# Performance work log

Measured on AMD Instinct MI355X. Metric: run time of the kernel, lower is better.

Reference implementation:

```python
import jax, jax.numpy as jnp
import numpy as np

IN_FEATURES = 4096
OUT_FEATURES = 768
N_BITS = 8
BATCH = 4096


def setup_inputs() -> dict:
    key = jax.random.key(0)
    k1, k2, k3 = jax.random.split(key, 3)
    latent = jax.random.uniform(k1, (BATCH, IN_FEATURES), dtype=jnp.float32)
    true_sum = jax.random.uniform(k2, (BATCH, OUT_FEATURES * N_BITS), dtype=jnp.float32)
    # kaiming-normal-ish init: std = sqrt(2 / fan_in)
    weight = jax.random.normal(k3, (IN_FEATURES, OUT_FEATURES * N_BITS), dtype=jnp.float32) * np.sqrt(2.0 / IN_FEATURES)
    return {"latent": latent, "true_sum": true_sum, "weight": weight, "n_bits": N_BITS}


def reference(latent, true_sum, weight, n_bits):
    in_features = weight.shape[0]
    batch = latent.shape[0]
    # powers of two, MSB negated (two's-complement style decode)
    powers = (2.0 ** jnp.arange(n_bits, dtype=jnp.float32))
    powers = powers.at[-1].multiply(-1.0)

    prob_weights = jax.nn.sigmoid(weight)                      # [in, out*n_bits]
    # decode soft bits -> integer-valued weights: [in, out]
    int_weights = (prob_weights.reshape(in_features, -1, n_bits) * powers).sum(-1)
    # decode target bits -> integer-valued sums: [batch, out]
    int_sum = (true_sum.reshape(batch, -1, n_bits) * powers).sum(-1)

    # (latent.unsqueeze(-1) * int_weights).sum(-2) is exactly a GEMM
    pred = latent @ int_weights                                # [batch, out]

    scale_factor = 2.0 ** (n_bits - 1)
    recon_loss = jnp.mean((pred - int_sum) ** 2) / scale_factor
    polarize_loss = jnp.mean(prob_weights * (1.0 - prob_weights))
    return (recon_loss, polarize_loss)
```

## Files before the change

kernel.cpp:

```cpp
#include <hip/hip_runtime.h>
#include <stdint.h>

#define IN_F   4096
#define OUT_F  768
#define NB     8
#define BATCH  4096
#define WCOLS  (OUT_F*NB)

typedef short  bf16x8  __attribute__((ext_vector_type(8)));
typedef float  f32x4   __attribute__((ext_vector_type(4)));
typedef unsigned short ushort8 __attribute__((ext_vector_type(8)));

__device__ __forceinline__ unsigned short f2bf(float f){
    union { float f; uint32_t u; } v; v.f = f;
    uint32_t u = v.u;
    u += 0x7FFFu + ((u >> 16) & 1u);
    return (unsigned short)(u >> 16);
}

__device__ __forceinline__ float bf2f(unsigned short u){
    union { uint32_t q; float f; } v; v.q = ((uint32_t)u) << 16;
    return v.f;
}

__device__ __forceinline__ void gload16(const void* g, void* l){
    __builtin_amdgcn_global_load_lds(
        (const __attribute__((address_space(1))) unsigned int*)g,
        (__attribute__((address_space(3))) unsigned int*)l, 16, 0, 0);
}

#define WAITV(n) do {                                                   \
    asm volatile("s_waitcnt vmcnt(" #n ")" ::: "memory");               \
    __builtin_amdgcn_sched_barrier(0);                                  \
} while (0)

__global__ void prep_latent(const float* __restrict__ lat,
                            unsigned short* __restrict__ abf,
                            float* __restrict__ acc){
    if (blockIdx.x == 0 && threadIdx.x < 4) acc[threadIdx.x] = 0.f;
    int idx = (blockIdx.x * 256 + threadIdx.x) * 8;
    const float4* p = (const float4*)(lat + idx);
    float4 a = p[0], b = p[1];
    ushort8 o;
    o[0]=f2bf(a.x); o[1]=f2bf(a.y); o[2]=f2bf(a.z); o[3]=f2bf(a.w);
    o[4]=f2bf(b.x); o[5]=f2bf(b.y); o[6]=f2bf(b.z); o[7]=f2bf(b.w);
    *(ushort8*)(abf + idx) = o;
}

__global__ void decode_weight(const float* __restrict__ w,
                              unsigned short* __restrict__ bt,
                              float* __restrict__ acc){
    __shared__ unsigned short tile[64][70];
    __shared__ float part[4];
    const int tid = threadIdx.x;
    const int k0 = blockIdx.x * 64;
    const int n0 = blockIdx.y * 64;
    const int j     = tid & 63;
    const int ibase = (tid >> 6) * 16;
    float pol = 0.f;
    #pragma unroll 4
    for (int r = 0; r < 16; ++r){
        int i = ibase + r;
        const float4* src = (const float4*)(w + (size_t)(k0+i)*WCOLS + (size_t)(n0+j)*8);
        float4 a = src[0], b = src[1];
        float x[8] = {a.x,a.y,a.z,a.w,b.x,b.y,b.z,b.w};
        float p[8];
        #pragma unroll
        for (int q = 0; q < 8; ++q){
            p[q] = 1.f / (1.f + __expf(-x[q]));
            pol += p[q] * (1.f - p[q]);
        }
        float iw = p[0] + 2.f*p[1] + 4.f*p[2] + 8.f*p[3]
                 + 16.f*p[4] + 32.f*p[5] + 64.f*p[6] - 128.f*p[7];
        tile[j][i] = f2bf(iw);
    }
    #pragma unroll
    for (int off = 32; off; off >>= 1) pol += __shfl_down(pol, off);
    if ((tid & 63) == 0) part[tid >> 6] = pol;
    __syncthreads();
    const int nrow = tid >> 4;
    const int kb   = (tid & 15) * 4;
    #pragma unroll
    for (int q = 0; q < 4; ++q){
        int n = nrow + q*16;
        uint2 v;
        v.x = *(const unsigned int*)&tile[n][kb];
        v.y = *(const unsigned int*)&tile[n][kb+2];
        *(uint2*)(bt + (size_t)(n0+n)*IN_F + k0 + kb) = v;
    }
    if (tid == 0) atomicAdd(&acc[1], part[0]+part[1]+part[2]+part[3]);
}

__global__ void ts_decode(const float* __restrict__ ts,
                          unsigned short* __restrict__ isum){
    const int tid = threadIdx.x;
    #pragma unroll
    for (int k = 0; k < 6; ++k){
        int e = blockIdx.x * 1536 + k * 256 + tid;
        const float4* q = (const float4*)(ts + (size_t)e * 8);
        float4 x = q[0], y = q[1];
        float v = x.x + 2.f*x.y + 4.f*x.z + 8.f*x.w
                + 16.f*y.x + 32.f*y.y + 64.f*y.z - 128.f*y.w;
        isum[e] = f2bf(v);
    }
}

#define BM 64
#define BN 96
#define BK 64
#define NT (IN_F/BK)
#define ABYTES (BM*BK*2)
#define BBYTES (BN*BK*2)
#define BUFB   (ABYTES+BBYTES)

__launch_bounds__(256, 2)
__global__ void gemm_loss(const unsigned short* __restrict__ abf,
                          const unsigned short* __restrict__ bt,
                          const unsigned short* __restrict__ isum,
                          float* __restrict__ acc){
    __shared__ char smem[3*BUFB];
    __shared__ float part[4];
    const int tid = threadIdx.x;
    const int w   = tid >> 6;
    const int l   = tid & 63;
    const int s   = l & 15, g = l >> 4;
    const int wr  = w >> 1, wc = w & 1;
    const int m0  = blockIdx.x * BM;
    const int n0  = blockIdx.y * BN;

    f32x4 accv[2][3];
    #pragma unroll
    for (int m = 0; m < 2; ++m)
        #pragma unroll
        for (int n = 0; n < 3; ++n)
            accv[m][n] = (f32x4){0.f,0.f,0.f,0.f};

    const int c8  = tid & 7;
    const int r0  = tid >> 3;
    const int scw = ((c8 ^ (r0 & 7)) << 3);
    const unsigned short* aS = abf + (size_t)(m0 + r0) * IN_F + scw;
    const unsigned short* bS = bt  + (size_t)(n0 + r0) * IN_F + scw;

    #define STAGE(kt, base) do {                                           \
        const int _ko = (kt) * BK;                                         \
        char* _ad = (base) + tid*16;                                       \
        char* _bd = (base) + ABYTES + tid*16;                              \
        gload16(aS + _ko,                      _ad);                       \
        gload16(aS + (size_t)32*IN_F + _ko,    _ad + 4096);                \
        gload16(bS + _ko,                      _bd);                       \
        gload16(bS + (size_t)32*IN_F + _ko,    _bd + 4096);                \
        gload16(bS + (size_t)64*IN_F + _ko,    _bd + 8192);                \
    } while (0)

    #define COMPUTE(base) do {                                             \
        char* _Ab = (base);                                                \
        char* _Bb = (base) + ABYTES;                                       \
        _Pragma("unroll")                                                  \
        for (int _kk = 0; _kk < 2; ++_kk){                                 \
            bf16x8 _af[2], _bf[3];                                         \
            _Pragma("unroll")                                              \
            for (int _m = 0; _m < 2; ++_m){                                \
                int _r  = wr*32 + _m*16 + s;                               \
                int _ch = _r*8 + ((_kk*4 + g) ^ (_r & 7));                 \
                _af[_m] = *(const bf16x8*)(_Ab + _ch*16);                  \
            }                                                              \
            _Pragma("unroll")                                              \
            for (int _n = 0; _n < 3; ++_n){                                \
                int _r  = wc*48 + _n*16 + s;                               \
                int _ch = _r*8 + ((_kk*4 + g) ^ (_r & 7));                 \
                _bf[_n] = *(const bf16x8*)(_Bb + _ch*16);                  \
            }                                                              \
            _Pragma("unroll")                                              \
            for (int _m = 0; _m < 2; ++_m)                                 \
                _Pragma("unroll")                                          \
                for (int _n = 0; _n < 3; ++_n)                             \
                    accv[_m][_n] = __builtin_amdgcn_mfma_f32_16x16x32_bf16(\
                        _af[_m], _bf[_n], accv[_m][_n], 0, 0, 0);          \
        }                                                                  \
    } while (0)

    char* p0 = smem;
    char* p1 = smem + BUFB;
    char* p2 = smem + 2*BUFB;

    STAGE(0, p0);
    STAGE(1, p1);
    for (int t = 0; t < NT-1; ++t){
        WAITV(5);
        __builtin_amdgcn_s_barrier();
        if (t + 2 < NT) STAGE(t + 2, p2);
        COMPUTE(p0);
        char* tmp = p0; p0 = p1; p1 = p2; p2 = tmp;
    }
    WAITV(0);
    __builtin_amdgcn_s_barrier();
    COMPUTE(p0);

    float local = 0.f;
    #pragma unroll
    for (int m = 0; m < 2; ++m){
        int rbase = m0 + wr*32 + m*16 + g*4;
        #pragma unroll
        for (int n = 0; n < 3; ++n){
            int col = n0 + wc*48 + n*16 + s;
            #pragma unroll
            for (int jj = 0; jj < 4; ++jj){
                float is = bf2f(isum[(size_t)(rbase+jj)*OUT_F + col]);
                float d = accv[m][n][jj] - is;
                local += d*d;
            }
        }
    }
    #pragma unroll
    for (int off = 32; off; off >>= 1) local += __shfl_down(local, off);
    if (l == 0) part[w] = local;
    __syncthreads();
    if (tid == 0){
        atomicAdd(&acc[0], part[0]+part[1]+part[2]+part[3]);
    }
}

__global__ void finalize(const float* __restrict__ acc, float* __restrict__ out){
    out[0] = acc[0] * (1.0f / ((float)BATCH * (float)OUT_F * 128.0f));
    out[1] = acc[1] * (1.0f / ((float)IN_F * (float)WCOLS));
}

extern "C" void kernel_launch(void* const* d_in, const int* in_sizes, int n_in,
                              void* d_out, int out_size, void* d_ws, size_t ws_size,
                              hipStream_t stream){
    const float* latent   = (const float*)d_in[0];
    const float* true_sum = (const float*)d_in[1];
    const float* weight   = (const float*)d_in[2];
    float* acc = (float*)d_ws;
    unsigned short* abf  = (unsigned short*)((char*)d_ws + 1024);
    unsigned short* bt   = (unsigned short*)((char*)d_ws + 1024 + (size_t)BATCH*IN_F*2);
    unsigned short* isum = (unsigned short*)((char*)d_ws + 1024 + (size_t)BATCH*IN_F*2
                                             + (size_t)OUT_F*IN_F*2);
    float* out = (float*)d_out;

    prep_latent<<<(BATCH*IN_F)/(256*8), 256, 0, stream>>>(latent, abf, acc);
    decode_weight<<<dim3(IN_F/64, OUT_F/64), 256, 0, stream>>>(weight, bt, acc);
    ts_decode<<<(BATCH*OUT_F)/(256*6), 256, 0, stream>>>(true_sum, isum);
    gemm_loss<<<dim3(BATCH/BM, OUT_F/BN), 256, 0, stream>>>(abf, bt, isum, acc);
    finalize<<<1, 1, 0, stream>>>(acc, out);
}
```

Before: 105.5 us.

## Warp-specialize GEMM into producer load waves and consumer MFMA waves

The GEMM block grows to 512 threads. Four waves only issue global-to-LDS loads into the triple buffer, and four waves only run MFMA, with the two groups synchronised by block barriers. The grid becomes 1D with n varying fastest so neighbouring blocks share A rows, and the compute waves raise their priority around the MFMA issue. This aims to hide load latency behind compute, at the cost of doubling threads per block, which may limit occupancy under the 4-blocks launch bound, and of idle producer waves during the epilogue.

```diff
diff --git a/kernel.cpp b/kernel.cpp
--- a/kernel.cpp
+++ b/kernel.cpp
@@ -113,20 +113,21 @@
 #define BBYTES (BN*BK*2)
 #define BUFB   (ABYTES+BBYTES)
 
-__launch_bounds__(256, 2)
+__launch_bounds__(512, 4)
 __global__ void gemm_loss(const unsigned short* __restrict__ abf,
                           const unsigned short* __restrict__ bt,
                           const unsigned short* __restrict__ isum,
                           float* __restrict__ acc){
     __shared__ char smem[3*BUFB];
-    __shared__ float part[4];
+    __shared__ float part[8];
     const int tid = threadIdx.x;
     const int w   = tid >> 6;
     const int l   = tid & 63;
     const int s   = l & 15, g = l >> 4;
     const int wr  = w >> 1, wc = w & 1;
-    const int m0  = blockIdx.x * BM;
-    const int n0  = blockIdx.y * BN;
+    const int bid = blockIdx.x;
+    const int m0  = (bid >> 3) * BM;
+    const int n0  = (bid & 7)  * BN;
 
     f32x4 accv[2][3];
     #pragma unroll
@@ -134,23 +135,6 @@
         #pragma unroll
         for (int n = 0; n < 3; ++n)
             accv[m][n] = (f32x4){0.f,0.f,0.f,0.f};
-
-    const int c8  = tid & 7;
-    const int r0  = tid >> 3;
-    const int scw = ((c8 ^ (r0 & 7)) << 3);
-    const unsigned short* aS = abf + (size_t)(m0 + r0) * IN_F + scw;
-    const unsigned short* bS = bt  + (size_t)(n0 + r0) * IN_F + scw;
-
-    #define STAGE(kt, base) do {                                           \
-        const int _ko = (kt) * BK;                                         \
-        char* _ad = (base) + tid*16;                                       \
-        char* _bd = (base) + ABYTES + tid*16;                              \
-        gload16(aS + _ko,                      _ad);                       \
-        gload16(aS + (size_t)32*IN_F + _ko,    _ad + 4096);                \
-        gload16(bS + _ko,                      _bd);                       \
-        gload16(bS + (size_t)32*IN_F + _ko,    _bd + 4096);                \
-        gload16(bS + (size_t)64*IN_F + _ko,    _bd + 8192);                \
-    } while (0)
 
     #define COMPUTE(base) do {                                             \
         char* _Ab = (base);                                                \
@@ -170,44 +154,78 @@
                 int _ch = _r*8 + ((_kk*4 + g) ^ (_r & 7));                 \
                 _bf[_n] = *(const bf16x8*)(_Bb + _ch*16);                  \
             }                                                              \
+            __builtin_amdgcn_s_setprio(1);                                 \
             _Pragma("unroll")                                              \
             for (int _m = 0; _m < 2; ++_m)                                 \
                 _Pragma("unroll")                                          \
                 for (int _n = 0; _n < 3; ++_n)                             \
                     accv[_m][_n] = __builtin_amdgcn_mfma_f32_16x16x32_bf16(\
                         _af[_m], _bf[_n], accv[_m][_n], 0, 0, 0);          \
+            __builtin_amdgcn_s_setprio(0);                                 \
         }                                                                  \
     } while (0)
 
-    char* p0 = smem;
-    char* p1 = smem + BUFB;
-    char* p2 = smem + 2*BUFB;
-
-    STAGE(0, p0);
-    STAGE(1, p1);
-    for (int t = 0; t < NT-1; ++t){
+    char* r0 = smem;
+    char* r1 = smem + BUFB;
+    char* r2 = smem + 2*BUFB;
+
+    if (w >= 4){
+        const int p  = w - 4;
+        const int lr = l >> 3;
+        const int lc = l & 7;
+        const unsigned short* src[5];
+        int dsto[5];
+        #pragma unroll
+        for (int i = 0; i < 5; ++i){
+            int c   = p + 4*i;
+            int row = (c < 8) ? (c*8 + lr) : ((c-8)*8 + lr);
+            int csw = ((lc ^ (row & 7)) << 3);
+            src[i]  = (c < 8) ? (abf + (size_t)(m0 + row)*IN_F + csw)
+                              : (bt  + (size_t)(n0 + row)*IN_F + csw);
+            dsto[i] = c * 1024;
+        }
+        #define STAGEP(kt, base) do {                                     \
+            _Pragma("unroll")                                             \
+            for (int _i = 0; _i < 5; ++_i)                                \
+                gload16(src[_i] + (size_t)(kt)*BK, (base) + dsto[_i]);    \
+        } while (0)
+
+        STAGEP(0, r0);
+        STAGEP(1, r1);
         WAITV(5);
         __builtin_amdgcn_s_barrier();
-        if (t + 2 < NT) STAGE(t + 2, p2);
-        COMPUTE(p0);
-        char* tmp = p0; p0 = p1; p1 = p2; p2 = tmp;
-    }
-    WAITV(0);
-    __builtin_amdgcn_s_barrier();
-    COMPUTE(p0);
+        for (int t = 0; t < NT; ++t){
+            __builtin_amdgcn_sched_barrier(0);
+            if (t < NT-2)      { STAGEP(t+2, r2); WAITV(5); }
+            else if (t == NT-2){ WAITV(0); }
+            __builtin_amdgcn_s_barrier();
+            char* tmp = r0; r0 = r1; r1 = r2; r2 = tmp;
+        }
+    } else {
+        __builtin_amdgcn_s_barrier();
+        for (int t = 0; t < NT; ++t){
+            __builtin_amdgcn_sched_barrier(0);
+            COMPUTE(r0);
+            __builtin_amdgcn_sched_barrier(0);
+            __builtin_amdgcn_s_barrier();
+            char* tmp = r0; r0 = r1; r1 = r2; r2 = tmp;
+        }
+    }
 
     float local = 0.f;
-    #pragma unroll
-    for (int m = 0; m < 2; ++m){
-        int rbase = m0 + wr*32 + m*16 + g*4;
-        #pragma unroll
-        for (int n = 0; n < 3; ++n){
-            int col = n0 + wc*48 + n*16 + s;
+    if (w < 4){
+        #pragma unroll
+        for (int m = 0; m < 2; ++m){
+            int rbase = m0 + wr*32 + m*16 + g*4;
             #pragma unroll
-            for (int jj = 0; jj < 4; ++jj){
-                float is = bf2f(isum[(size_t)(rbase+jj)*OUT_F + col]);
-                float d = accv[m][n][jj] - is;
-                local += d*d;
+            for (int n = 0; n < 3; ++n){
+                int col = n0 + wc*48 + n*16 + s;
+                #pragma unroll
+                for (int jj = 0; jj < 4; ++jj){
+                    float is = bf2f(isum[(size_t)(rbase+jj)*OUT_F + col]);
+                    float d = accv[m][n][jj] - is;
+                    local += d*d;
+                }
             }
         }
     }
@@ -216,7 +234,10 @@
     if (l == 0) part[w] = local;
     __syncthreads();
     if (tid == 0){
-        atomicAdd(&acc[0], part[0]+part[1]+part[2]+part[3]);
+        float ssum = 0.f;
+        #pragma unroll
+        for (int i = 0; i < 8; ++i) ssum += part[i];
+        atomicAdd(&acc[0], ssum);
     }
 }
 
@@ -241,6 +262,6 @@
     prep_latent<<<(BATCH*IN_F)/(256*8), 256, 0, stream>>>(latent, abf, acc);
     decode_weight<<<dim3(IN_F/64, OUT_F/64), 256, 0, stream>>>(weight, bt, acc);
     ts_decode<<<(BATCH*OUT_F)/(256*6), 256, 0, stream>>>(true_sum, isum);
-    gemm_loss<<<dim3(BATCH/BM, OUT_F/BN), 256, 0, stream>>>(abf, bt, isum, acc);
+    gemm_loss<<<BATCH/BM * OUT_F/BN, 512, 0, stream>>>(abf, bt, isum, acc);
     finalize<<<1, 1, 0, stream>>>(acc, out);
 }
```

Result: slower. 109.0 us (+3.3%).
